# Kernel tuning notes

Hardware: AMD Instinct MI355X
Metric: run time of the kernel (lower is better)

## Reference

```python
import jax, jax.numpy as jnp
import numpy as np

N_FEATURES = 784   # binary tabular features (MNIST-like)
Z_DIM = 64         # latent dim fed to decoder net
BX = 256           # number of data points x
BZ = 4096          # number of latent samples / components z


def setup_inputs() -> dict:
    key = jax.random.key(0)
    k1, k2, k3 = jax.random.split(key, 3)
    x = jax.random.uniform(k1, (BX, N_FEATURES), dtype=jnp.float32)  # soft targets in [0,1)
    z = jax.random.normal(k2, (BZ, Z_DIM), dtype=jnp.float32)
    # net := Linear(Z_DIM -> 2*N_FEATURES)
    W = jax.random.normal(k3, (Z_DIM, 2 * N_FEATURES), dtype=jnp.float32) * 0.05
    b = jnp.zeros((2 * N_FEATURES,), dtype=jnp.float32)
    # chain-structured CLT: root = feature 0 (parent -1), feature i's parent is i-1
    tree = jnp.concatenate([jnp.array([-1], dtype=jnp.int32),
                            jnp.arange(N_FEATURES - 1, dtype=jnp.int32)])
    return {"x": x, "z": z, "W": W, "b": b, "tree": tree}


def reference(x, z, W, b, tree):
    F = tree.shape[0]
    # net(z) -> logits_p [Bz, F, 2]
    logits_p = (z @ W + b).reshape(-1, F, 2)
    # _preprocess_logits_p: at root, copy state-1 logit into state-0 slot
    root_mask = (tree == -1)  # [F]
    lp0 = jnp.where(root_mask[None, :], logits_p[:, :, 1], logits_p[:, :, 0])
    logits_p = jnp.stack([lp0, logits_p[:, :, 1]], axis=-1)  # [Bz, F, 2]
    # parent-conditioned selector x_cond [Bx, F, 2]
    xt = x[:, tree]  # gather parent values; -1 at root wraps (same as torch)
    x_cond = jnp.stack([1.0 - xt, xt], axis=-1)
    # bce (negative binary cross-entropy = Bernoulli log-likelihood):
    #   lls[b,i,j,k] = x[b,j]*log_sigmoid(lp[i,j,k]) + (1-x[b,j])*log_sigmoid(-lp[i,j,k])
    # (x_doubled duplicates x along k, so both k slots use x[b,j])
    # Then einsum('bijk,bjk->bij', lls, x_cond).sum(-1). Distribute x_cond to
    # avoid materializing the [Bx,Bz,F,2] lls tensor (same math, fused):
    ls = jax.nn.log_sigmoid(logits_p)     # [Bz, F, 2]
    lsn = jax.nn.log_sigmoid(-logits_p)   # [Bz, F, 2]
    a = x_cond * x[:, :, None]            # [Bx, F, 2]
    c = x_cond * (1.0 - x)[:, :, None]    # [Bx, F, 2]
    log_prob_bins = (jnp.einsum('bjk,ijk->bi', a, ls)
                     + jnp.einsum('bjk,ijk->bi', c, lsn))  # [Bx, Bz]
    return log_prob_bins
```

## Files before the change

kernel.cpp:

```cpp
#include <hip/hip_runtime.h>

#define NF   784
#define ZD   64
#define BXN  256
#define BZN  4096
#define KDIM 3136
#define LCOL 1568

typedef __attribute__((ext_vector_type(8))) short bf16x8;
typedef __attribute__((ext_vector_type(4))) float f32x4;
typedef __attribute__((ext_vector_type(8))) unsigned short ushort8;

__device__ __forceinline__ unsigned short f2bf(float f) {
  unsigned u = __float_as_uint(f);
  u += 0x7fff + ((u >> 16) & 1);
  return (unsigned short)(u >> 16);
}

__global__ __launch_bounds__(256) void prep(const float* __restrict__ x,
                                            const float* __restrict__ z,
                                            const float* __restrict__ W,
                                            const int* __restrict__ tree,
                                            unsigned short* __restrict__ Amat,
                                            unsigned short* __restrict__ zb,
                                            unsigned short* __restrict__ Wt) {
  int bid = blockIdx.x, tid = threadIdx.x;
  if (bid < 1024) {
    int b = bid >> 2;
    int j = (bid & 3) * 256 + tid;
    if (j >= NF) return;
    float xb = x[b * NF + j];
    int idx = tree[j];
    int gidx = idx < 0 ? idx + NF : idx;
    float xt = x[b * NF + gidx];
    ushort4 v;
    v.x = f2bf((1.f - xt) * xb);
    v.y = f2bf(xt * xb);
    v.z = f2bf((1.f - xt) * (1.f - xb));
    v.w = f2bf(xt * (1.f - xb));
    *(ushort4*)&Amat[(size_t)b * KDIM + 4 * j] = v;
  } else if (bid < 1280) {
    int t = (bid - 1024) * 256 + tid;
    float4 v = *(const float4*)&z[t * 4];
    ushort4 o = { f2bf(v.x), f2bf(v.y), f2bf(v.z), f2bf(v.w) };
    *(ushort4*)&zb[t * 4] = o;
  } else {
    int t = (bid - 1280) * 256 + tid;
    int c = t >> 4, k0 = (t & 15) * 4;
    ushort4 o;
    o.x = f2bf(W[(k0 + 0) * LCOL + c]);
    o.y = f2bf(W[(k0 + 1) * LCOL + c]);
    o.z = f2bf(W[(k0 + 2) * LCOL + c]);
    o.w = f2bf(W[(k0 + 3) * LCOL + c]);
    *(ushort4*)&Wt[c * 64 + k0] = o;
  }
}

#define LP 40
__global__ __launch_bounds__(256) void gemm_fused(const unsigned short* __restrict__ Amat,
                                                  const unsigned short* __restrict__ zb,
                                                  const unsigned short* __restrict__ Wt,
                                                  const float* __restrict__ bias,
                                                  const int* __restrict__ tree,
                                                  float* __restrict__ part) {
  __shared__ unsigned short As[2][256][LP];
  __shared__ unsigned short Bs[2][64][LP];
  int bid = blockIdx.x;
  int s = bid & 7, nt = bid >> 3;
  int n0 = nt * 64;
  int kt0 = s * 12 + (s < 2 ? s : 2);
  int nsteps = (s < 2) ? 13 : 12;
  int ktend = kt0 + nsteps;
  int tid = threadIdx.x;
  int w = tid >> 6, lane = tid & 63;
  int fr = lane & 15, hi = lane >> 4, kq = hi * 8;
  int srow = tid >> 2, scol = (tid & 3) * 8;
  const unsigned short* Ag = Amat + (size_t)srow * KDIM + scol;

  const unsigned short* zp = zb + (size_t)(n0 + w * 16 + fr) * 64 + kq;
  bf16x8 zf0 = *(const bf16x8*)zp;
  bf16x8 zf1 = *(const bf16x8*)(zp + 32);

  f32x4 acc[4][4];
#pragma unroll
  for (int m = 0; m < 4; ++m)
#pragma unroll
    for (int n = 0; n < 4; ++n) acc[m][n] = (f32x4){0.f, 0.f, 0.f, 0.f};

  const unsigned short* wp = Wt + (size_t)(kt0 * 16 + fr) * 64 + kq;
  bf16x8 wf0 = *(const bf16x8*)wp;
  bf16x8 wf1 = *(const bf16x8*)(wp + 32);
  float4 b4  = *(const float4*)&bias[kt0 * 16 + 4 * hi];
  int2   tr2 = *(const int2*)&tree[kt0 * 8 + 2 * hi];
  int k0 = kt0 * 32;
  float4 ar0 = *(const float4*)(Ag + k0);
  float4 ar1 = *(const float4*)(Ag + (size_t)64 * KDIM + k0);
  float4 ar2 = *(const float4*)(Ag + (size_t)128 * KDIM + k0);
  float4 ar3 = *(const float4*)(Ag + (size_t)192 * KDIM + k0);

  int buf = 0;
  for (int i = 0; i < nsteps; ++i) {
    int kt = kt0 + i;
    f32x4 lacc = (f32x4){0.f, 0.f, 0.f, 0.f};
    lacc = __builtin_amdgcn_mfma_f32_16x16x32_bf16(wf0, zf0, lacc, 0, 0, 0);
    lacc = __builtin_amdgcn_mfma_f32_16x16x32_bf16(wf1, zf1, lacc, 0, 0, 0);
    int ktn = (kt + 1 < ktend) ? kt + 1 : kt;
    const unsigned short* wpn = Wt + (size_t)(ktn * 16 + fr) * 64 + kq;
    bf16x8 wfn0 = *(const bf16x8*)wpn;
    bf16x8 wfn1 = *(const bf16x8*)(wpn + 32);
    float4 b4n  = *(const float4*)&bias[ktn * 16 + 4 * hi];
    int2   tr2n = *(const int2*)&tree[ktn * 8 + 2 * hi];
    int k0n = ktn * 32;
    float4 arn0 = *(const float4*)(Ag + k0n);
    float4 arn1 = *(const float4*)(Ag + (size_t)64 * KDIM + k0n);
    float4 arn2 = *(const float4*)(Ag + (size_t)128 * KDIM + k0n);
    float4 arn3 = *(const float4*)(Ag + (size_t)192 * KDIM + k0n);
    float bb[4] = { b4.x, b4.y, b4.z, b4.w };
    int tt[2] = { tr2.x, tr2.y };
    ushort8 v;
#pragma unroll
    for (int p = 0; p < 2; ++p) {
      float l1 = lacc[2 * p + 1] + bb[2 * p + 1];
      float l0 = (tt[p] == -1) ? l1 : (lacc[2 * p] + bb[2 * p]);
      float e0 = __expf(-fabsf(l0)); float sp0 = __logf(1.f + e0);
      float ls0 = (l0 >= 0.f) ? -sp0 : l0 - sp0;
      float e1 = __expf(-fabsf(l1)); float sp1 = __logf(1.f + e1);
      float ls1 = (l1 >= 0.f) ? -sp1 : l1 - sp1;
      v[4 * p + 0] = f2bf(ls0);
      v[4 * p + 1] = f2bf(ls1);
      v[4 * p + 2] = f2bf(ls0 - l0);
      v[4 * p + 3] = f2bf(ls1 - l1);
    }
    *(float4*)&As[buf][srow      ][scol] = ar0;
    *(float4*)&As[buf][srow +  64][scol] = ar1;
    *(float4*)&As[buf][srow + 128][scol] = ar2;
    *(float4*)&As[buf][srow + 192][scol] = ar3;
    *(ushort8*)&Bs[buf][w * 16 + fr][kq] = v;
    __syncthreads();
    bf16x8 a[4], b[4];
#pragma unroll
    for (int m = 0; m < 4; ++m) a[m] = *(const bf16x8*)&As[buf][w * 64 + m * 16 + fr][kq];
#pragma unroll
    for (int n = 0; n < 4; ++n) b[n] = *(const bf16x8*)&Bs[buf][n * 16 + fr][kq];
#pragma unroll
    for (int m = 0; m < 4; ++m)
#pragma unroll
      for (int n = 0; n < 4; ++n)
        acc[m][n] = __builtin_amdgcn_mfma_f32_16x16x32_bf16(a[m], b[n], acc[m][n], 0, 0, 0);
    wf0 = wfn0; wf1 = wfn1; b4 = b4n; tr2 = tr2n;
    ar0 = arn0; ar1 = arn1; ar2 = arn2; ar3 = arn3;
    buf ^= 1;
  }
  int col = lane & 15, rq = hi * 4;
  float* Pp = part + (size_t)s * (256 * 4096) + (size_t)(w * 64) * 4096 + n0;
#pragma unroll
  for (int m = 0; m < 4; ++m)
#pragma unroll
    for (int n = 0; n < 4; ++n)
#pragma unroll
      for (int r = 0; r < 4; ++r)
        __builtin_nontemporal_store(acc[m][n][r],
                                    &Pp[(m * 16 + rq + r) * 4096 + n * 16 + col]);
}

__global__ __launch_bounds__(256) void reduce8(const float* __restrict__ part,
                                               float* __restrict__ out) {
  int t = blockIdx.x * 256 + threadIdx.x;
  f32x4 s = (f32x4){0.f, 0.f, 0.f, 0.f};
#pragma unroll
  for (int q = 0; q < 8; ++q) {
    const f32x4* p = (const f32x4*)&part[(size_t)q * (256 * 4096) + (size_t)t * 4];
    s += __builtin_nontemporal_load(p);
  }
  f32x4* o = (f32x4*)&out[(size_t)t * 4];
  __builtin_nontemporal_store(s, o);
}

extern "C" void kernel_launch(void* const* d_in, const int* in_sizes, int n_in,
                              void* d_out, int out_size, void* d_ws, size_t ws_size,
                              hipStream_t stream) {
  const float* x    = (const float*)d_in[0];
  const float* z    = (const float*)d_in[1];
  const float* W    = (const float*)d_in[2];
  const float* bias = (const float*)d_in[3];
  const int*   tree = (const int*)d_in[4];
  float* out = (float*)d_out;

  unsigned short* Amat = (unsigned short*)d_ws;
  unsigned short* zb   = (unsigned short*)((char*)d_ws + 1605632);
  unsigned short* Wt   = (unsigned short*)((char*)d_ws + 2129920);
  float*          part = (float*)((char*)d_ws + 2330624);

  prep<<<dim3(1378), 256, 0, stream>>>(x, z, W, tree, Amat, zb, Wt);
  gemm_fused<<<dim3(512), 256, 0, stream>>>(Amat, zb, Wt, bias, tree, part);
  reduce8<<<dim3(1024), 256, 0, stream>>>(part, out);
}
```

Measured before the change: 42.89 us.

## Load A fragments directly into registers and double K-step per iteration

The GEMM now loads each wave's A-operand MFMA fragments straight from global memory into registers, so the A tile no longer passes through shared memory. Each iteration covers 64 K-columns instead of 32 (two logit column groups), which halves the number of barriers and loop trips. Launch bounds request two blocks per CU. In exchange, per-lane global loads become strided 16-byte reads across rows and register pressure rises, which could spill under the occupancy hint.

```diff
diff --git a/kernel.cpp b/kernel.cpp
--- a/kernel.cpp
+++ b/kernel.cpp
@@ -56,102 +56,123 @@
   }
 }
 
-#define LP 40
-__global__ __launch_bounds__(256) void gemm_fused(const unsigned short* __restrict__ Amat,
-                                                  const unsigned short* __restrict__ zb,
-                                                  const unsigned short* __restrict__ Wt,
-                                                  const float* __restrict__ bias,
-                                                  const int* __restrict__ tree,
-                                                  float* __restrict__ part) {
-  __shared__ unsigned short As[2][256][LP];
-  __shared__ unsigned short Bs[2][64][LP];
+#define LPB 72
+__global__ __launch_bounds__(256, 2) void gemm_fused(const unsigned short* __restrict__ Amat,
+                                                     const unsigned short* __restrict__ zb,
+                                                     const unsigned short* __restrict__ Wt,
+                                                     const float* __restrict__ bias,
+                                                     const int* __restrict__ tree,
+                                                     float* __restrict__ part) {
+  __shared__ unsigned short Bs[2][64][LPB];
   int bid = blockIdx.x;
   int s = bid & 7, nt = bid >> 3;
   int n0 = nt * 64;
-  int kt0 = s * 12 + (s < 2 ? s : 2);
-  int nsteps = (s < 2) ? 13 : 12;
+  int kt0    = (s == 0) ? 0 : 7 + 6 * (s - 1);
+  int nsteps = (s == 0) ? 7 : 6;
   int ktend = kt0 + nsteps;
   int tid = threadIdx.x;
   int w = tid >> 6, lane = tid & 63;
   int fr = lane & 15, hi = lane >> 4, kq = hi * 8;
-  int srow = tid >> 2, scol = (tid & 3) * 8;
-  const unsigned short* Ag = Amat + (size_t)srow * KDIM + scol;
 
   const unsigned short* zp = zb + (size_t)(n0 + w * 16 + fr) * 64 + kq;
   bf16x8 zf0 = *(const bf16x8*)zp;
   bf16x8 zf1 = *(const bf16x8*)(zp + 32);
 
+  const unsigned short* Agf = Amat + (size_t)(w * 64 + fr) * KDIM + kq;
+
   f32x4 acc[4][4];
 #pragma unroll
   for (int m = 0; m < 4; ++m)
 #pragma unroll
     for (int n = 0; n < 4; ++n) acc[m][n] = (f32x4){0.f, 0.f, 0.f, 0.f};
 
-  const unsigned short* wp = Wt + (size_t)(kt0 * 16 + fr) * 64 + kq;
-  bf16x8 wf0 = *(const bf16x8*)wp;
-  bf16x8 wf1 = *(const bf16x8*)(wp + 32);
-  float4 b4  = *(const float4*)&bias[kt0 * 16 + 4 * hi];
-  int2   tr2 = *(const int2*)&tree[kt0 * 8 + 2 * hi];
-  int k0 = kt0 * 32;
-  float4 ar0 = *(const float4*)(Ag + k0);
-  float4 ar1 = *(const float4*)(Ag + (size_t)64 * KDIM + k0);
-  float4 ar2 = *(const float4*)(Ag + (size_t)128 * KDIM + k0);
-  float4 ar3 = *(const float4*)(Ag + (size_t)192 * KDIM + k0);
+  bf16x8 wfc[2][2]; float4 b4c[2]; int2 trc[2];
+#pragma unroll
+  for (int cg = 0; cg < 2; ++cg) {
+    const unsigned short* wp = Wt + (size_t)(kt0 * 32 + cg * 16 + fr) * 64 + kq;
+    wfc[cg][0] = *(const bf16x8*)wp;
+    wfc[cg][1] = *(const bf16x8*)(wp + 32);
+    b4c[cg] = *(const float4*)&bias[kt0 * 32 + cg * 16 + 4 * hi];
+    trc[cg] = *(const int2*)&tree[kt0 * 16 + cg * 8 + 2 * hi];
+  }
+  bf16x8 ac[4][2];
+#pragma unroll
+  for (int m = 0; m < 4; ++m)
+#pragma unroll
+    for (int kc = 0; kc < 2; ++kc)
+      ac[m][kc] = *(const bf16x8*)(Agf + (size_t)m * 16 * KDIM + kt0 * 64 + kc * 32);
 
   int buf = 0;
   for (int i = 0; i < nsteps; ++i) {
     int kt = kt0 + i;
-    f32x4 lacc = (f32x4){0.f, 0.f, 0.f, 0.f};
-    lacc = __builtin_amdgcn_mfma_f32_16x16x32_bf16(wf0, zf0, lacc, 0, 0, 0);
-    lacc = __builtin_amdgcn_mfma_f32_16x16x32_bf16(wf1, zf1, lacc, 0, 0, 0);
+    f32x4 lacc[2];
+#pragma unroll
+    for (int cg = 0; cg < 2; ++cg) {
+      lacc[cg] = (f32x4){0.f, 0.f, 0.f, 0.f};
+      lacc[cg] = __builtin_amdgcn_mfma_f32_16x16x32_bf16(wfc[cg][0], zf0, lacc[cg], 0, 0, 0);
+      lacc[cg] = __builtin_amdgcn_mfma_f32_16x16x32_bf16(wfc[cg][1], zf1, lacc[cg], 0, 0, 0);
+    }
     int ktn = (kt + 1 < ktend) ? kt + 1 : kt;
-    const unsigned short* wpn = Wt + (size_t)(ktn * 16 + fr) * 64 + kq;
-    bf16x8 wfn0 = *(const bf16x8*)wpn;
-    bf16x8 wfn1 = *(const bf16x8*)(wpn + 32);
-    float4 b4n  = *(const float4*)&bias[ktn * 16 + 4 * hi];
-    int2   tr2n = *(const int2*)&tree[ktn * 8 + 2 * hi];
-    int k0n = ktn * 32;
-    float4 arn0 = *(const float4*)(Ag + k0n);
-    float4 arn1 = *(const float4*)(Ag + (size_t)64 * KDIM + k0n);
-    float4 arn2 = *(const float4*)(Ag + (size_t)128 * KDIM + k0n);
-    float4 arn3 = *(const float4*)(Ag + (size_t)192 * KDIM + k0n);
-    float bb[4] = { b4.x, b4.y, b4.z, b4.w };
-    int tt[2] = { tr2.x, tr2.y };
-    ushort8 v;
-#pragma unroll
-    for (int p = 0; p < 2; ++p) {
-      float l1 = lacc[2 * p + 1] + bb[2 * p + 1];
-      float l0 = (tt[p] == -1) ? l1 : (lacc[2 * p] + bb[2 * p]);
-      float e0 = __expf(-fabsf(l0)); float sp0 = __logf(1.f + e0);
-      float ls0 = (l0 >= 0.f) ? -sp0 : l0 - sp0;
-      float e1 = __expf(-fabsf(l1)); float sp1 = __logf(1.f + e1);
-      float ls1 = (l1 >= 0.f) ? -sp1 : l1 - sp1;
-      v[4 * p + 0] = f2bf(ls0);
-      v[4 * p + 1] = f2bf(ls1);
-      v[4 * p + 2] = f2bf(ls0 - l0);
-      v[4 * p + 3] = f2bf(ls1 - l1);
-    }
-    *(float4*)&As[buf][srow      ][scol] = ar0;
-    *(float4*)&As[buf][srow +  64][scol] = ar1;
-    *(float4*)&As[buf][srow + 128][scol] = ar2;
-    *(float4*)&As[buf][srow + 192][scol] = ar3;
-    *(ushort8*)&Bs[buf][w * 16 + fr][kq] = v;
+    bf16x8 wfn[2][2]; float4 b4n[2]; int2 trn[2];
+#pragma unroll
+    for (int cg = 0; cg < 2; ++cg) {
+      const unsigned short* wpn = Wt + (size_t)(ktn * 32 + cg * 16 + fr) * 64 + kq;
+      wfn[cg][0] = *(const bf16x8*)wpn;
+      wfn[cg][1] = *(const bf16x8*)(wpn + 32);
+      b4n[cg] = *(const float4*)&bias[ktn * 32 + cg * 16 + 4 * hi];
+      trn[cg] = *(const int2*)&tree[ktn * 16 + cg * 8 + 2 * hi];
+    }
+    bf16x8 an[4][2];
+#pragma unroll
+    for (int m = 0; m < 4; ++m)
+#pragma unroll
+      for (int kc = 0; kc < 2; ++kc)
+        an[m][kc] = *(const bf16x8*)(Agf + (size_t)m * 16 * KDIM + ktn * 64 + kc * 32);
+#pragma unroll
+    for (int cg = 0; cg < 2; ++cg) {
+      float bb[4] = { b4c[cg].x, b4c[cg].y, b4c[cg].z, b4c[cg].w };
+      int tt[2] = { trc[cg].x, trc[cg].y };
+      ushort8 v;
+#pragma unroll
+      for (int p = 0; p < 2; ++p) {
+        float l1 = lacc[cg][2 * p + 1] + bb[2 * p + 1];
+        float l0 = (tt[p] == -1) ? l1 : (lacc[cg][2 * p] + bb[2 * p]);
+        float e0 = __expf(-fabsf(l0)); float sp0 = __logf(1.f + e0);
+        float ls0 = (l0 >= 0.f) ? -sp0 : l0 - sp0;
+        float e1 = __expf(-fabsf(l1)); float sp1 = __logf(1.f + e1);
+        float ls1 = (l1 >= 0.f) ? -sp1 : l1 - sp1;
+        v[4 * p + 0] = f2bf(ls0);
+        v[4 * p + 1] = f2bf(ls1);
+        v[4 * p + 2] = f2bf(ls0 - l0);
+        v[4 * p + 3] = f2bf(ls1 - l1);
+      }
+      *(ushort8*)&Bs[buf][w * 16 + fr][cg * 32 + kq] = v;
+    }
     __syncthreads();
-    bf16x8 a[4], b[4];
-#pragma unroll
-    for (int m = 0; m < 4; ++m) a[m] = *(const bf16x8*)&As[buf][w * 64 + m * 16 + fr][kq];
-#pragma unroll
-    for (int n = 0; n < 4; ++n) b[n] = *(const bf16x8*)&Bs[buf][n * 16 + fr][kq];
-#pragma unroll
-    for (int m = 0; m < 4; ++m)
+#pragma unroll
+    for (int kc = 0; kc < 2; ++kc) {
+      bf16x8 b[4];
 #pragma unroll
       for (int n = 0; n < 4; ++n)
-        acc[m][n] = __builtin_amdgcn_mfma_f32_16x16x32_bf16(a[m], b[n], acc[m][n], 0, 0, 0);
-    wf0 = wfn0; wf1 = wfn1; b4 = b4n; tr2 = tr2n;
-    ar0 = arn0; ar1 = arn1; ar2 = arn2; ar3 = arn3;
+        b[n] = *(const bf16x8*)&Bs[buf][n * 16 + fr][kc * 32 + kq];
+#pragma unroll
+      for (int m = 0; m < 4; ++m)
+#pragma unroll
+        for (int n = 0; n < 4; ++n)
+          acc[m][n] = __builtin_amdgcn_mfma_f32_16x16x32_bf16(ac[m][kc], b[n], acc[m][n], 0, 0, 0);
+    }
+#pragma unroll
+    for (int cg = 0; cg < 2; ++cg) {
+      wfc[cg][0] = wfn[cg][0]; wfc[cg][1] = wfn[cg][1];
+      b4c[cg] = b4n[cg]; trc[cg] = trn[cg];
+    }
+#pragma unroll
+    for (int m = 0; m < 4; ++m) {
+      ac[m][0] = an[m][0]; ac[m][1] = an[m][1];
+    }
     buf ^= 1;
   }
-  int col = lane & 15, rq = hi * 4;
+  int rq = hi * 4;
   float* Pp = part + (size_t)s * (256 * 4096) + (size_t)(w * 64) * 4096 + n0;
 #pragma unroll
   for (int m = 0; m < 4; ++m)
@@ -160,7 +181,7 @@
 #pragma unroll
       for (int r = 0; r < 4; ++r)
         __builtin_nontemporal_store(acc[m][n][r],
-                                    &Pp[(m * 16 + rq + r) * 4096 + n * 16 + col]);
+                                    &Pp[(m * 16 + rq + r) * 4096 + n * 16 + fr]);
 }
 
 __global__ __launch_bounds__(256) void reduce8(const float* __restrict__ part,
```

Result: slower. 47.24 us (+10.1%).
